# Kernel optimization log

Measured on AMD Instinct MI355X. Metric: run time of the kernel, lower is better.

## Reference

```python
import jax, jax.numpy as jnp
import numpy as np

N = 1048576          # total nodes
HID = 256            # hidden_dim
G = 2048             # number of graphs (batch.max()+1)


def setup_inputs() -> dict:
    key = jax.random.key(0)
    k1, k2, k3, k4 = jax.random.split(key, 4)
    x = jax.random.normal(k1, (N, HID), dtype=jnp.float32)
    batch = jnp.sort(jax.random.randint(k2, (N,), 0, G)).astype(jnp.int64)
    W1 = jax.random.normal(k3, (HID, HID // 2), dtype=jnp.float32) * (1.0 / np.sqrt(HID))
    b1 = jnp.zeros((HID // 2,), dtype=jnp.float32)
    W2 = jax.random.normal(k4, (HID // 2, 1), dtype=jnp.float32) * (1.0 / np.sqrt(HID // 2))
    b2 = jnp.zeros((1,), dtype=jnp.float32)
    return {"x": x, "batch": batch, "W1": W1, "b1": b1, "W2": W2, "b2": b2}


def reference(x, batch, W1, b1, W2, b2):
    # attention scores: small MLP -> scalar per node
    h = jnp.tanh(x @ W1 + b1)                  # [N, HID/2]
    scores = (h @ W2 + b2)[:, 0]               # [N]
    # per-graph (segment) softmax, numerically stable
    seg_max = jax.ops.segment_max(scores, batch, num_segments=G)   # [G]
    ex = jnp.exp(scores - seg_max[batch])                           # [N]
    denom = jax.ops.segment_sum(ex, batch, num_segments=G)          # [G]
    w = ex / denom[batch]                                           # [N]
    # weighted sum of node features per graph
    pooled = jax.ops.segment_sum(x * w[:, None], batch, num_segments=G)  # [G, HID]
    return pooled
```

## Files before the change

### kernel.cpp

```cpp
#include <hip/hip_runtime.h>


#define HID   256
#define HHID  128
#define TILE  128
#define BLK   512
#define PITCH 264

typedef __attribute__((ext_vector_type(8))) short short8;
typedef __attribute__((ext_vector_type(4))) float f32x4;

__device__ __forceinline__ unsigned short f2bf(float f) {
  unsigned u = __builtin_bit_cast(unsigned, f);
  u += 0x7fffu + ((u >> 16) & 1u);
  return (unsigned short)(u >> 16);
}
__device__ __forceinline__ float bf2f(unsigned short s) {
  unsigned u = ((unsigned)s) << 16;
  return __builtin_bit_cast(float, u);
}

__global__ void prep_kernel(const float* __restrict__ W1,
                            const int* __restrict__ batch,
                            unsigned short* __restrict__ w1t,
                            int* __restrict__ starts,
                            int n, int g) {
  int tid = blockIdx.x * blockDim.x + threadIdx.x;
  if (tid < HID * HHID) {
    int k = tid / HHID, j = tid % HHID;
    w1t[j * HID + k] = f2bf(W1[tid]);
  }
  if (tid < n) {
    int b = batch[tid];
    int prev = (tid == 0) ? -1 : batch[tid - 1];
    for (int q = prev + 1; q <= b; ++q) starts[q] = tid;
    if (tid == n - 1)
      for (int q = b + 1; q <= g; ++q) starts[q] = n;
  }
}

__global__ __launch_bounds__(BLK, 2) void pool_kernel(
    const float* __restrict__ x,
    const int* __restrict__ starts,
    const float* __restrict__ b1,
    const float* __restrict__ W2,
    const float* __restrict__ b2,
    const unsigned short* __restrict__ w1t,
    float* __restrict__ out)
{
  __shared__ __align__(16) unsigned short lds_w1t[HHID * PITCH];
  __shared__ __align__(16) unsigned short lds_x[TILE * PITCH];
  __shared__ float lds_sc[TILE];
  __shared__ float lds_b1[HHID];
  __shared__ float lds_w2[HHID];
  __shared__ float lds_state[4];

  const int t    = threadIdx.x;
  const int g    = blockIdx.x;
  const int lane = t & 63;
  const int wave = t >> 6;

  for (int i = t; i < (HHID * HID) / 8; i += BLK) {
    int row = i >> 5, c8 = (i & 31) << 3;
    short8 v = *(const short8*)(w1t + row * HID + c8);
    *(short8*)(&lds_w1t[row * PITCH + c8]) = v;
  }
  if (t < HHID) { lds_b1[t] = b1[t]; lds_w2[t] = W2[t]; }
  if (t == 0)   { lds_state[0] = -1e30f; lds_state[1] = 0.f; lds_state[2] = 0.f; }

  const int start = starts[g], end = starts[g + 1];
  const int cnt = end - start;
  const float b2v = b2[0];

  const int cg = (t & 31) << 3;
  const int sl = t >> 5;
  float opart[8];
#pragma unroll
  for (int j = 0; j < 8; ++j) opart[j] = 0.f;

  __syncthreads();

  if (cnt > 0) {
    const int ntiles = (cnt + TILE - 1) / TILE;
    f32x4 pre[16];

    auto load_tile = [&](int tbase) {
#pragma unroll
      for (int k2 = 0; k2 < 8; ++k2) {
        int item = t + k2 * BLK;
        int row  = item >> 5;
        int c8   = (item & 31) << 3;
        int node = start + tbase + row;
        if (node < end) {
          const float* p = x + (size_t)node * HID + c8;
          pre[2 * k2]     = *(const f32x4*)p;
          pre[2 * k2 + 1] = *(const f32x4*)(p + 4);
        } else {
          pre[2 * k2]     = (f32x4){0.f, 0.f, 0.f, 0.f};
          pre[2 * k2 + 1] = (f32x4){0.f, 0.f, 0.f, 0.f};
        }
      }
    };

    load_tile(0);

    for (int tb = 0; tb < ntiles; ++tb) {
      const int tbase = tb * TILE;

      __syncthreads();
#pragma unroll
      for (int k2 = 0; k2 < 8; ++k2) {
        int item = t + k2 * BLK;
        int row  = item >> 5;
        int c8   = (item & 31) << 3;
        short8 v;
#pragma unroll
        for (int q = 0; q < 8; ++q) {
          float f = (q < 4) ? pre[2 * k2][q] : pre[2 * k2 + 1][q - 4];
          v[q] = (short)f2bf(f);
        }
        *(short8*)(&lds_x[row * PITCH + c8]) = v;
      }
      __syncthreads();

      if (tb + 1 < ntiles) load_tile(tbase + TILE);

      short8 afrag[8];
      const int arow = wave * 16 + (lane & 15);
      const int kq   = (lane >> 4) << 3;
#pragma unroll
      for (int s = 0; s < 8; ++s)
        afrag[s] = *(const short8*)(&lds_x[arow * PITCH + s * 32 + kq]);

      float p[4] = {0.f, 0.f, 0.f, 0.f};
      const int bj = lane & 15;
#pragma unroll
      for (int c = 0; c < 8; ++c) {
        f32x4 acc = {0.f, 0.f, 0.f, 0.f};
#pragma unroll
        for (int s = 0; s < 8; ++s) {
          short8 bfrag = *(const short8*)(&lds_w1t[(c * 16 + bj) * PITCH + s * 32 + kq]);
          acc = __builtin_amdgcn_mfma_f32_16x16x32_bf16(afrag[s], bfrag, acc, 0, 0, 0);
        }
        int col = c * 16 + bj;
        float b1v = lds_b1[col], w2v = lds_w2[col];
#pragma unroll
        for (int r = 0; r < 4; ++r) {
          float h  = acc[r] + b1v;
          float e2 = __expf(2.f * h);
          float th = (e2 - 1.f) / (e2 + 1.f);
          p[r] += th * w2v;
        }
      }
#pragma unroll
      for (int m = 1; m <= 8; m <<= 1) {
#pragma unroll
        for (int r = 0; r < 4; ++r) p[r] += __shfl_xor(p[r], m, 64);
      }
      {
        int r = lane & 15;
        if (r < 4) {
          int nl = wave * 16 + ((lane >> 4) << 2) + r;
          float pr = (r == 0) ? p[0] : (r == 1) ? p[1] : (r == 2) ? p[2] : p[3];
          int node = start + tbase + nl;
          lds_sc[nl] = (node < end) ? (pr + b2v) : -1e30f;
        }
      }
      __syncthreads();

      if (wave == 0) {
        float s0 = lds_sc[lane], s1 = lds_sc[lane + 64];
        float mx = fmaxf(s0, s1);
#pragma unroll
        for (int m = 1; m <= 32; m <<= 1) mx = fmaxf(mx, __shfl_xor(mx, m, 64));
        float mold = lds_state[0];
        float mnew = fmaxf(mold, mx);
        float alpha = __expf(mold - mnew);
        float e0 = __expf(s0 - mnew), e1 = __expf(s1 - mnew);
        lds_sc[lane] = e0; lds_sc[lane + 64] = e1;
        float es = e0 + e1;
#pragma unroll
        for (int m = 1; m <= 32; m <<= 1) es += __shfl_xor(es, m, 64);
        if (lane == 0) {
          lds_state[1] = lds_state[1] * alpha + es;
          lds_state[0] = mnew;
          lds_state[2] = alpha;
        }
      }
      __syncthreads();

      {
        float alpha = lds_state[2];
#pragma unroll
        for (int j = 0; j < 8; ++j) opart[j] *= alpha;
#pragma unroll
        for (int it = 0; it < TILE / 16; ++it) {
          int n = sl + it * 16;
          float e = lds_sc[n];
          short8 xv = *(const short8*)(&lds_x[n * PITCH + cg]);
#pragma unroll
          for (int j = 0; j < 8; ++j)
            opart[j] = fmaf(e, bf2f((unsigned short)xv[j]), opart[j]);
        }
      }
    }
  }

  __syncthreads();
  float* red = (float*)lds_x;
  {
    f32x4 a = {opart[0], opart[1], opart[2], opart[3]};
    f32x4 b = {opart[4], opart[5], opart[6], opart[7]};
    *(f32x4*)(&red[sl * HID + cg])     = a;
    *(f32x4*)(&red[sl * HID + cg + 4]) = b;
  }
  __syncthreads();
#pragma unroll
  for (int st = 8; st >= 1; st >>= 1) {
    if (sl < st) {
#pragma unroll
      for (int j = 0; j < 8; ++j)
        red[sl * HID + cg + j] += red[(sl + st) * HID + cg + j];
    }
    __syncthreads();
  }
  if (t < 64) {
    float l = lds_state[1];
    float inv = (cnt > 0) ? 1.f / l : 0.f;
    f32x4 o;
#pragma unroll
    for (int j = 0; j < 4; ++j) o[j] = red[t * 4 + j] * inv;
    *(f32x4*)(out + (size_t)g * HID + t * 4) = o;
  }
}

extern "C" void kernel_launch(void* const* d_in, const int* in_sizes, int n_in,
                              void* d_out, int out_size, void* d_ws, size_t ws_size,
                              hipStream_t stream) {
  const float* x     = (const float*)d_in[0];
  const int*   batch = (const int*)d_in[1];
  const float* W1    = (const float*)d_in[2];
  const float* b1    = (const float*)d_in[3];
  const float* W2    = (const float*)d_in[4];
  const float* b2    = (const float*)d_in[5];
  float* out = (float*)d_out;

  const int n = in_sizes[0] / HID;
  const int g = out_size / HID;

  unsigned short* w1t = (unsigned short*)d_ws;
  int* starts = (int*)((char*)d_ws + (size_t)HID * HHID * sizeof(unsigned short));

  prep_kernel<<<(n + 255) / 256, 256, 0, stream>>>(W1, batch, w1t, starts, n, g);
  pool_kernel<<<g, BLK, 0, stream>>>(x, starts, b1, W2, b2, w1t, out);
}
```

Measured before the change: 1.434 ms.

## Split fused per-graph pool into score, segment-softmax, and pooling kernels

Replaces the single per-graph fused kernel, which ran the MLP, an online softmax and pooling inside one block per graph, with three kernels. A grid-stride score kernel keeps W1 fragments in registers, a small per-graph kernel computes the max and inverse sum, and a pooling kernel reads x again in fp32. The aim is to remove per-block W1 loading, the serial per-tile syncs and the imbalance between graphs of different sizes, and to raise occupancy. In exchange x is read from HBM twice, and the pooling now uses fp32 x instead of the bf16 copy.

```diff
diff --git a/kernel.cpp b/kernel.cpp
--- a/kernel.cpp
+++ b/kernel.cpp
@@ -14,10 +14,6 @@
   unsigned u = __builtin_bit_cast(unsigned, f);
   u += 0x7fffu + ((u >> 16) & 1u);
   return (unsigned short)(u >> 16);
-}
-__device__ __forceinline__ float bf2f(unsigned short s) {
-  unsigned u = ((unsigned)s) << 16;
-  return __builtin_bit_cast(float, u);
 }
 
 __global__ void prep_kernel(const float* __restrict__ W1,
@@ -39,181 +35,164 @@
   }
 }
 
-__global__ __launch_bounds__(BLK, 2) void pool_kernel(
+__global__ __launch_bounds__(BLK, 4) void score_kernel(
     const float* __restrict__ x,
-    const int* __restrict__ starts,
+    const unsigned short* __restrict__ w1t,
     const float* __restrict__ b1,
     const float* __restrict__ W2,
     const float* __restrict__ b2,
-    const unsigned short* __restrict__ w1t,
+    float* __restrict__ scores,
+    int n)
+{
+  __shared__ __align__(16) unsigned short lds_x[TILE * PITCH];
+  __shared__ float lds_part[8][TILE];
+
+  const int t    = threadIdx.x;
+  const int lane = t & 63;
+  const int wave = t >> 6;
+  const int col  = wave * 16 + (lane & 15);
+  const int kq   = (lane >> 4) << 3;
+  const int hi   = lane >> 4;
+
+  short8 bfrag[8];
+#pragma unroll
+  for (int s = 0; s < 8; ++s)
+    bfrag[s] = *(const short8*)(w1t + col * HID + s * 32 + kq);
+  const float b1v = b1[col];
+  const float w2v = W2[col];
+  const float b2v = b2[0];
+
+  const int ntiles = (n + TILE - 1) / TILE;
+
+  for (int tt = blockIdx.x; tt < ntiles; tt += gridDim.x) {
+    const int base = tt * TILE;
+
+    __syncthreads();
+
+#pragma unroll
+    for (int k2 = 0; k2 < 8; ++k2) {
+      int item = t + k2 * BLK;
+      int row  = item >> 5;
+      int c8   = (item & 31) << 3;
+      int node = base + row;
+      f32x4 a, b;
+      if (node < n) {
+        const float* p = x + (size_t)node * HID + c8;
+        a = *(const f32x4*)p;
+        b = *(const f32x4*)(p + 4);
+      } else {
+        a = (f32x4){0.f, 0.f, 0.f, 0.f};
+        b = a;
+      }
+      short8 v;
+#pragma unroll
+      for (int q = 0; q < 4; ++q) v[q]     = (short)f2bf(a[q]);
+#pragma unroll
+      for (int q = 0; q < 4; ++q) v[q + 4] = (short)f2bf(b[q]);
+      *(short8*)(&lds_x[row * PITCH + c8]) = v;
+    }
+    __syncthreads();
+
+#pragma unroll
+    for (int rt = 0; rt < 8; ++rt) {
+      const int arow = rt * 16 + (lane & 15);
+      f32x4 acc = {0.f, 0.f, 0.f, 0.f};
+#pragma unroll
+      for (int s = 0; s < 8; ++s) {
+        short8 afrag = *(const short8*)(&lds_x[arow * PITCH + s * 32 + kq]);
+        acc = __builtin_amdgcn_mfma_f32_16x16x32_bf16(afrag, bfrag[s], acc, 0, 0, 0);
+      }
+      float p[4];
+#pragma unroll
+      for (int r = 0; r < 4; ++r) {
+        float h  = acc[r] + b1v;
+        float e2 = __expf(2.f * h);
+        float th = (e2 - 1.f) / (e2 + 1.f);
+        p[r] = th * w2v;
+      }
+#pragma unroll
+      for (int m = 1; m <= 8; m <<= 1) {
+#pragma unroll
+        for (int r = 0; r < 4; ++r) p[r] += __shfl_xor(p[r], m, 64);
+      }
+      if ((lane & 15) == 0) {
+#pragma unroll
+        for (int r = 0; r < 4; ++r)
+          lds_part[wave][rt * 16 + hi * 4 + r] = p[r];
+      }
+    }
+    __syncthreads();
+
+    if (t < TILE) {
+      float s = b2v;
+#pragma unroll
+      for (int w = 0; w < 8; ++w) s += lds_part[w][t];
+      int node = base + t;
+      if (node < n) scores[node] = s;
+    }
+  }
+}
+
+__global__ void seg_kernel(const float* __restrict__ scores,
+                           const int* __restrict__ starts,
+                           float* __restrict__ mg,
+                           float* __restrict__ invl)
+{
+  const int g    = blockIdx.x;
+  const int lane = threadIdx.x;
+  const int s0 = starts[g], s1 = starts[g + 1];
+
+  float mx = -1e30f;
+  for (int i = s0 + lane; i < s1; i += 64) mx = fmaxf(mx, scores[i]);
+#pragma unroll
+  for (int m = 1; m <= 32; m <<= 1) mx = fmaxf(mx, __shfl_xor(mx, m, 64));
+
+  float sum = 0.f;
+  for (int i = s0 + lane; i < s1; i += 64) sum += __expf(scores[i] - mx);
+#pragma unroll
+  for (int m = 1; m <= 32; m <<= 1) sum += __shfl_xor(sum, m, 64);
+
+  if (lane == 0) {
+    mg[g]   = mx;
+    invl[g] = (s1 > s0) ? 1.f / sum : 0.f;
+  }
+}
+
+__global__ __launch_bounds__(BLK, 8) void pool2_kernel(
+    const float* __restrict__ x,
+    const float* __restrict__ scores,
+    const int* __restrict__ starts,
+    const float* __restrict__ mg,
+    const float* __restrict__ invl,
     float* __restrict__ out)
 {
-  __shared__ __align__(16) unsigned short lds_w1t[HHID * PITCH];
-  __shared__ __align__(16) unsigned short lds_x[TILE * PITCH];
-  __shared__ float lds_sc[TILE];
-  __shared__ float lds_b1[HHID];
-  __shared__ float lds_w2[HHID];
-  __shared__ float lds_state[4];
-
-  const int t    = threadIdx.x;
-  const int g    = blockIdx.x;
-  const int lane = t & 63;
-  const int wave = t >> 6;
-
-  for (int i = t; i < (HHID * HID) / 8; i += BLK) {
-    int row = i >> 5, c8 = (i & 31) << 3;
-    short8 v = *(const short8*)(w1t + row * HID + c8);
-    *(short8*)(&lds_w1t[row * PITCH + c8]) = v;
-  }
-  if (t < HHID) { lds_b1[t] = b1[t]; lds_w2[t] = W2[t]; }
-  if (t == 0)   { lds_state[0] = -1e30f; lds_state[1] = 0.f; lds_state[2] = 0.f; }
-
+  __shared__ __align__(16) float red[16 * HID];
+
+  const int t  = threadIdx.x;
+  const int g  = blockIdx.x;
   const int start = starts[g], end = starts[g + 1];
-  const int cnt = end - start;
-  const float b2v = b2[0];
-
+  const float m  = mg[g];
+  const float il = invl[g];
   const int cg = (t & 31) << 3;
   const int sl = t >> 5;
-  float opart[8];
-#pragma unroll
-  for (int j = 0; j < 8; ++j) opart[j] = 0.f;
-
-  __syncthreads();
-
-  if (cnt > 0) {
-    const int ntiles = (cnt + TILE - 1) / TILE;
-    f32x4 pre[16];
-
-    auto load_tile = [&](int tbase) {
-#pragma unroll
-      for (int k2 = 0; k2 < 8; ++k2) {
-        int item = t + k2 * BLK;
-        int row  = item >> 5;
-        int c8   = (item & 31) << 3;
-        int node = start + tbase + row;
-        if (node < end) {
-          const float* p = x + (size_t)node * HID + c8;
-          pre[2 * k2]     = *(const f32x4*)p;
-          pre[2 * k2 + 1] = *(const f32x4*)(p + 4);
-        } else {
-          pre[2 * k2]     = (f32x4){0.f, 0.f, 0.f, 0.f};
-          pre[2 * k2 + 1] = (f32x4){0.f, 0.f, 0.f, 0.f};
-        }
-      }
-    };
-
-    load_tile(0);
-
-    for (int tb = 0; tb < ntiles; ++tb) {
-      const int tbase = tb * TILE;
-
-      __syncthreads();
-#pragma unroll
-      for (int k2 = 0; k2 < 8; ++k2) {
-        int item = t + k2 * BLK;
-        int row  = item >> 5;
-        int c8   = (item & 31) << 3;
-        short8 v;
-#pragma unroll
-        for (int q = 0; q < 8; ++q) {
-          float f = (q < 4) ? pre[2 * k2][q] : pre[2 * k2 + 1][q - 4];
-          v[q] = (short)f2bf(f);
-        }
-        *(short8*)(&lds_x[row * PITCH + c8]) = v;
-      }
-      __syncthreads();
-
-      if (tb + 1 < ntiles) load_tile(tbase + TILE);
-
-      short8 afrag[8];
-      const int arow = wave * 16 + (lane & 15);
-      const int kq   = (lane >> 4) << 3;
-#pragma unroll
-      for (int s = 0; s < 8; ++s)
-        afrag[s] = *(const short8*)(&lds_x[arow * PITCH + s * 32 + kq]);
-
-      float p[4] = {0.f, 0.f, 0.f, 0.f};
-      const int bj = lane & 15;
-#pragma unroll
-      for (int c = 0; c < 8; ++c) {
-        f32x4 acc = {0.f, 0.f, 0.f, 0.f};
-#pragma unroll
-        for (int s = 0; s < 8; ++s) {
-          short8 bfrag = *(const short8*)(&lds_w1t[(c * 16 + bj) * PITCH + s * 32 + kq]);
-          acc = __builtin_amdgcn_mfma_f32_16x16x32_bf16(afrag[s], bfrag, acc, 0, 0, 0);
-        }
-        int col = c * 16 + bj;
-        float b1v = lds_b1[col], w2v = lds_w2[col];
-#pragma unroll
-        for (int r = 0; r < 4; ++r) {
-          float h  = acc[r] + b1v;
-          float e2 = __expf(2.f * h);
-          float th = (e2 - 1.f) / (e2 + 1.f);
-          p[r] += th * w2v;
-        }
-      }
-#pragma unroll
-      for (int m = 1; m <= 8; m <<= 1) {
-#pragma unroll
-        for (int r = 0; r < 4; ++r) p[r] += __shfl_xor(p[r], m, 64);
-      }
-      {
-        int r = lane & 15;
-        if (r < 4) {
-          int nl = wave * 16 + ((lane >> 4) << 2) + r;
-          float pr = (r == 0) ? p[0] : (r == 1) ? p[1] : (r == 2) ? p[2] : p[3];
-          int node = start + tbase + nl;
-          lds_sc[nl] = (node < end) ? (pr + b2v) : -1e30f;
-        }
-      }
-      __syncthreads();
-
-      if (wave == 0) {
-        float s0 = lds_sc[lane], s1 = lds_sc[lane + 64];
-        float mx = fmaxf(s0, s1);
-#pragma unroll
-        for (int m = 1; m <= 32; m <<= 1) mx = fmaxf(mx, __shfl_xor(mx, m, 64));
-        float mold = lds_state[0];
-        float mnew = fmaxf(mold, mx);
-        float alpha = __expf(mold - mnew);
-        float e0 = __expf(s0 - mnew), e1 = __expf(s1 - mnew);
-        lds_sc[lane] = e0; lds_sc[lane + 64] = e1;
-        float es = e0 + e1;
-#pragma unroll
-        for (int m = 1; m <= 32; m <<= 1) es += __shfl_xor(es, m, 64);
-        if (lane == 0) {
-          lds_state[1] = lds_state[1] * alpha + es;
-          lds_state[0] = mnew;
-          lds_state[2] = alpha;
-        }
-      }
-      __syncthreads();
-
-      {
-        float alpha = lds_state[2];
-#pragma unroll
-        for (int j = 0; j < 8; ++j) opart[j] *= alpha;
-#pragma unroll
-        for (int it = 0; it < TILE / 16; ++it) {
-          int n = sl + it * 16;
-          float e = lds_sc[n];
-          short8 xv = *(const short8*)(&lds_x[n * PITCH + cg]);
-#pragma unroll
-          for (int j = 0; j < 8; ++j)
-            opart[j] = fmaf(e, bf2f((unsigned short)xv[j]), opart[j]);
-        }
-      }
-    }
-  }
-
-  __syncthreads();
-  float* red = (float*)lds_x;
-  {
-    f32x4 a = {opart[0], opart[1], opart[2], opart[3]};
-    f32x4 b = {opart[4], opart[5], opart[6], opart[7]};
-    *(f32x4*)(&red[sl * HID + cg])     = a;
-    *(f32x4*)(&red[sl * HID + cg + 4]) = b;
-  }
+
+  f32x4 oa = {0.f, 0.f, 0.f, 0.f};
+  f32x4 ob = {0.f, 0.f, 0.f, 0.f};
+
+  for (int nd = start + sl; nd < end; nd += 16) {
+    float w = __expf(scores[nd] - m);
+    const float* p = x + (size_t)nd * HID + cg;
+    f32x4 a = *(const f32x4*)p;
+    f32x4 b = *(const f32x4*)(p + 4);
+#pragma unroll
+    for (int j = 0; j < 4; ++j) {
+      oa[j] = fmaf(w, a[j], oa[j]);
+      ob[j] = fmaf(w, b[j], ob[j]);
+    }
+  }
+
+  *(f32x4*)(&red[sl * HID + cg])     = oa;
+  *(f32x4*)(&red[sl * HID + cg + 4]) = ob;
   __syncthreads();
 #pragma unroll
   for (int st = 8; st >= 1; st >>= 1) {
@@ -225,11 +204,9 @@
     __syncthreads();
   }
   if (t < 64) {
-    float l = lds_state[1];
-    float inv = (cnt > 0) ? 1.f / l : 0.f;
     f32x4 o;
 #pragma unroll
-    for (int j = 0; j < 4; ++j) o[j] = red[t * 4 + j] * inv;
+    for (int j = 0; j < 4; ++j) o[j] = red[t * 4 + j] * il;
     *(f32x4*)(out + (size_t)g * HID + t * 4) = o;
   }
 }
@@ -249,8 +226,13 @@
   const int g = out_size / HID;
 
   unsigned short* w1t = (unsigned short*)d_ws;
-  int* starts = (int*)((char*)d_ws + (size_t)HID * HHID * sizeof(unsigned short));
+  int*   starts = (int*)((char*)d_ws + 65536);
+  float* scores = (float*)((char*)d_ws + 65536 + 8448);
+  float* mg     = scores + n;
+  float* invl   = mg + g;
 
   prep_kernel<<<(n + 255) / 256, 256, 0, stream>>>(W1, batch, w1t, starts, n, g);
-  pool_kernel<<<g, BLK, 0, stream>>>(x, starts, b1, W2, b2, w1t, out);
-}
+  score_kernel<<<2048, BLK, 0, stream>>>(x, w1t, b1, W2, b2, scores, n);
+  seg_kernel<<<g, 64, 0, stream>>>(scores, starts, mg, invl);
+  pool2_kernel<<<g, BLK, 0, stream>>>(x, scores, starts, mg, invl, out);
+}
```

After: 1.597 ms. +11.4%, slower.
